# Performance work log

Hardware: AMD Instinct MI355X
Metric: run time of the kernel (lower is better)

Reference implementation:

```python
import jax, jax.numpy as jnp
import numpy as np

N_TOKENS = 16384
D_MODEL = 1024
N_SEG = 4
H_SEG = 1024  # intermediate_size (4096) // num_segments


def setup_inputs() -> dict:
    key = jax.random.key(0)
    kx, ki, kg, ku, kd = jax.random.split(key, 5)
    x = jax.random.normal(kx, (N_TOKENS, D_MODEL), dtype=jnp.float32)
    token_segment_indices = jax.random.randint(ki, (N_TOKENS,), 0, N_SEG, dtype=jnp.int64)
    s = 1.0 / np.sqrt(D_MODEL)
    # weights stored [seg, in, out] for x @ W
    gate_w = jax.random.normal(kg, (N_SEG, D_MODEL, H_SEG), dtype=jnp.float32) * s
    up_w = jax.random.normal(ku, (N_SEG, D_MODEL, H_SEG), dtype=jnp.float32) * s
    down_w = jax.random.normal(kd, (N_SEG, H_SEG, D_MODEL), dtype=jnp.float32) * (1.0 / np.sqrt(H_SEG))
    return {
        'x': x,
        'gate_w': gate_w,
        'up_w': up_w,
        'down_w': down_w,
        'token_segment_indices': token_segment_indices,
    }


def reference(x, gate_w, up_w, down_w, token_segment_indices):
    # _forward_with_indices: each token is processed only by its assigned
    # segment's SwiGLU FFN; all other contributions are zero.  We compute each
    # segment densely and mask (jit-friendly, same math as gather->ffn->scatter).
    out = jnp.zeros_like(x)
    for s in range(N_SEG):
        hidden = jax.nn.silu(x @ gate_w[s]) * (x @ up_w[s])  # [N, H_SEG]
        y = hidden @ down_w[s]                                # [N, D_MODEL]
        mask = (token_segment_indices == s)[:, None]
        out = out + jnp.where(mask, y, 0.0)
    return out
```

## Files before the change

kernel.cpp:

```cpp
#include <hip/hip_runtime.h>
#include <hip/hip_bf16.h>
#include <math.h>

#define NT   16384
#define DM   1024
#define NSEG 4
#define BK   64
#define HS   1024

typedef __attribute__((ext_vector_type(8))) short bf16x8;
typedef __attribute__((ext_vector_type(4))) float f32x4;

typedef __attribute__((address_space(1))) unsigned int gu32;
typedef __attribute__((address_space(3))) unsigned int lu32;

__device__ __forceinline__ void gll16(const void* g, void* l) {
  __builtin_amdgcn_global_load_lds((gu32*)(unsigned long long)g,
                                   (lu32*)(unsigned int)(unsigned long long)l,
                                   16, 0, 0);
}

__device__ __forceinline__ unsigned short cvt_bf16(float f) {
  unsigned int u = __float_as_uint(f);
  u += 0x7fffu + ((u >> 16) & 1u);
  return (unsigned short)(u >> 16);
}


__global__ void k_init(int* meta) {
  if (threadIdx.x < 16) meta[threadIdx.x] = 0;
}

__global__ void k_detect(const int* __restrict__ idx32, int* meta) {
  int t = blockIdx.x * 256 + threadIdx.x;
  int lane = threadIdx.x & 63;
  unsigned long long m = __ballot(idx32[2 * t + 1] != 0);
  if (lane == 0 && m) atomicOr(&meta[4], 1);
}

__global__ void k_count(const int* __restrict__ idx, int* meta) {
  int t = blockIdx.x * 256 + threadIdx.x;
  int s = meta[4] ? idx[t] : idx[2 * t];
  int lane = threadIdx.x & 63;
#pragma unroll
  for (int q = 0; q < 4; ++q) {
    unsigned long long m = __ballot(s == q);
    if (lane == 0 && m) atomicAdd(&meta[q], (int)__popcll(m));
  }
}

__global__ void k_base(int* meta) {
  int c0 = meta[0], c1 = meta[1], c2 = meta[2];
  meta[5] = 0; meta[6] = c0; meta[7] = c0 + c1; meta[8] = c0 + c1 + c2;
  meta[9] = 0; meta[10] = c0; meta[11] = c0 + c1; meta[12] = c0 + c1 + c2;
}

__global__ void k_rank(const int* __restrict__ idx, int* meta,
                       int* __restrict__ rank, int* __restrict__ perm) {
  int t = blockIdx.x * 256 + threadIdx.x;
  int s = meta[4] ? idx[t] : idx[2 * t];
  int lane = threadIdx.x & 63;
  unsigned long long lt = (1ull << lane) - 1;
#pragma unroll
  for (int q = 0; q < 4; ++q) {
    unsigned long long m = __ballot(s == q);
    int wb = 0;
    if (lane == 0 && m) wb = atomicAdd(&meta[9 + q], (int)__popcll(m));
    wb = __shfl(wb, 0);
    if (s == q) {
      int r = wb + (int)__popcll(m & lt);
      rank[t] = r;
      perm[r] = t;
    }
  }
}

__global__ __launch_bounds__(256) void k_cvt_x(const float4* __restrict__ x,
                                               const int* __restrict__ rank,
                                               uint4* __restrict__ xc) {
  int tid = threadIdx.x;
  int tok = blockIdx.x * 2 + (tid >> 7);
  int li = tid & 127;
  int r = rank[tok];
  float4 a = x[tok * 256 + li * 2];
  float4 b = x[tok * 256 + li * 2 + 1];
  uint4 o;
  o.x = cvt_bf16(a.x) | ((unsigned)cvt_bf16(a.y) << 16);
  o.y = cvt_bf16(a.z) | ((unsigned)cvt_bf16(a.w) << 16);
  o.z = cvt_bf16(b.x) | ((unsigned)cvt_bf16(b.y) << 16);
  o.w = cvt_bf16(b.z) | ((unsigned)cvt_bf16(b.w) << 16);
  xc[r * 128 + li] = o;
}

__global__ __launch_bounds__(256) void k_trans_w(
    const float* __restrict__ gw, const float* __restrict__ uw, const float* __restrict__ dw,
    unsigned short* __restrict__ gwt, unsigned short* __restrict__ uwt,
    unsigned short* __restrict__ dwt) {
  __shared__ float tile[64][65];
  int z = blockIdx.z, mtx = z >> 2, s = z & 3;
  const float* src = (mtx == 0 ? gw : mtx == 1 ? uw : dw) + (size_t)s * DM * HS;
  unsigned short* dst = (mtx == 0 ? gwt : mtx == 1 ? uwt : dwt) + (size_t)s * DM * HS;
  int k0 = blockIdx.y * 64, n0 = blockIdx.x * 64;
  int col = threadIdx.x & 63, rb = threadIdx.x >> 6;
#pragma unroll
  for (int i = 0; i < 64; i += 4)
    tile[i + rb][col] = src[(size_t)(k0 + i + rb) * 1024 + n0 + col];
  __syncthreads();
  int kp = threadIdx.x & 31, nb = threadIdx.x >> 5;
#pragma unroll
  for (int j = 0; j < 64; j += 8) {
    int nn = j + nb;
    unsigned int w = (unsigned)cvt_bf16(tile[2 * kp][nn]) |
                     ((unsigned)cvt_bf16(tile[2 * kp + 1][nn]) << 16);
    *(unsigned int*)(dst + (size_t)(n0 + nn) * 1024 + k0 + 2 * kp) = w;
  }
}

__global__ __launch_bounds__(256) void k_gateup(
    const unsigned short* __restrict__ xc,
    const unsigned short* __restrict__ gwt,
    const unsigned short* __restrict__ uwt,
    const int* __restrict__ meta,
    unsigned short* __restrict__ hidden) {
  const int seg = blockIdx.z;
  const int count = meta[seg];
  const int m0 = blockIdx.y * 128;
  if (m0 >= count) return;
  const int base = meta[5 + seg];
  const int n0 = blockIdx.x * 64;

  __shared__ __align__(16) unsigned short As[128 * BK];
  __shared__ __align__(16) unsigned short Bg[64 * BK];
  __shared__ __align__(16) unsigned short Bu[64 * BK];

  const int tid = threadIdx.x;
  const int lane = tid & 63;
  const int wave = tid >> 6;

  int a_off[4];
#pragma unroll
  for (int is = 0; is < 4; ++is) {
    int c = is * 256 + tid;
    int m = c >> 3;
    int kb = (c & 7) ^ (m & 7);
    int row = m0 + m;
    row = row < count ? row : count - 1;
    a_off[is] = (base + row) * DM + kb * 8;
  }
  int b_off[2];
#pragma unroll
  for (int is = 0; is < 2; ++is) {
    int c = is * 256 + tid;
    int n = c >> 3;
    int kb = (c & 7) ^ (n & 7);
    b_off[is] = (seg * HS + n0 + n) * DM + kb * 8;
  }

  f32x4 accg[4][2] = {};
  f32x4 accu[4][2] = {};
  const int wm = (wave & 1) * 64;
  const int wn = (wave >> 1) * 32;
  const int fm = lane & 15;
  const int fq = lane >> 4;
  const int fx = lane & 7;

  for (int kt = 0; kt < DM / BK; ++kt) {
    const int k0 = kt * BK;
    __syncthreads();
#pragma unroll
    for (int is = 0; is < 4; ++is)
      gll16(xc + a_off[is] + k0, (char*)As + (is * 256 + wave * 64) * 16);
#pragma unroll
    for (int is = 0; is < 2; ++is) {
      gll16(gwt + b_off[is] + k0, (char*)Bg + (is * 256 + wave * 64) * 16);
      gll16(uwt + b_off[is] + k0, (char*)Bu + (is * 256 + wave * 64) * 16);
    }
    __syncthreads();
#pragma unroll
    for (int s = 0; s < 2; ++s) {
      bf16x8 af[4], bgf[2], buf_[2];
      const int kb = (s * 4 + fq) ^ fx;
#pragma unroll
      for (int mi = 0; mi < 4; ++mi)
        af[mi] = *(const bf16x8*)((const char*)As + (((wm + mi * 16 + fm) * 8) + kb) * 16);
#pragma unroll
      for (int ni = 0; ni < 2; ++ni) {
        bgf[ni] = *(const bf16x8*)((const char*)Bg + (((wn + ni * 16 + fm) * 8) + kb) * 16);
        buf_[ni] = *(const bf16x8*)((const char*)Bu + (((wn + ni * 16 + fm) * 8) + kb) * 16);
      }
#pragma unroll
      for (int mi = 0; mi < 4; ++mi)
#pragma unroll
        for (int ni = 0; ni < 2; ++ni) {
          accg[mi][ni] = __builtin_amdgcn_mfma_f32_16x16x32_bf16(af[mi], bgf[ni], accg[mi][ni], 0, 0, 0);
          accu[mi][ni] = __builtin_amdgcn_mfma_f32_16x16x32_bf16(af[mi], buf_[ni], accu[mi][ni], 0, 0, 0);
        }
    }
  }

  const int rq = fq * 4;
#pragma unroll
  for (int mi = 0; mi < 4; ++mi) {
#pragma unroll
    for (int r = 0; r < 4; ++r) {
      int row = m0 + wm + mi * 16 + rq + r;
      if (row < count) {
        unsigned short* h = hidden + (size_t)(base + row) * HS + n0 + wn;
#pragma unroll
        for (int ni = 0; ni < 2; ++ni) {
          float g = accg[mi][ni][r];
          float u = accu[mi][ni][r];
          float sig = 1.0f / (1.0f + __expf(-g));
          h[ni * 16 + fm] = cvt_bf16(g * sig * u);
        }
      }
    }
  }
}

__global__ __launch_bounds__(256) void k_down(
    const unsigned short* __restrict__ hidden,
    const unsigned short* __restrict__ dwt,
    const int* __restrict__ meta,
    const int* __restrict__ perm,
    float* __restrict__ out) {
  const int seg = blockIdx.z;
  const int count = meta[seg];
  const int m0 = blockIdx.y * 128;
  if (m0 >= count) return;
  const int base = meta[5 + seg];
  const int n0 = blockIdx.x * 128;

  __shared__ __align__(16) unsigned short As[128 * BK];
  __shared__ __align__(16) unsigned short Bs[128 * BK];

  const int tid = threadIdx.x;
  const int lane = tid & 63;
  const int wave = tid >> 6;

  int a_off[4], b_off[4];
#pragma unroll
  for (int is = 0; is < 4; ++is) {
    int c = is * 256 + tid;
    int m = c >> 3;
    int kb = (c & 7) ^ (m & 7);
    int row = m0 + m;
    row = row < count ? row : count - 1;
    a_off[is] = (base + row) * HS + kb * 8;
    b_off[is] = (seg * DM + n0 + m) * HS + kb * 8;
  }

  f32x4 acc[4][4] = {};
  const int wm = (wave & 1) * 64;
  const int wn = (wave >> 1) * 64;
  const int fm = lane & 15;
  const int fq = lane >> 4;
  const int fx = lane & 7;

  for (int kt = 0; kt < HS / BK; ++kt) {
    const int k0 = kt * BK;
    __syncthreads();
#pragma unroll
    for (int is = 0; is < 4; ++is) {
      gll16(hidden + a_off[is] + k0, (char*)As + (is * 256 + wave * 64) * 16);
      gll16(dwt + b_off[is] + k0, (char*)Bs + (is * 256 + wave * 64) * 16);
    }
    __syncthreads();
#pragma unroll
    for (int s = 0; s < 2; ++s) {
      bf16x8 af[4], bf[4];
      const int kb = (s * 4 + fq) ^ fx;
#pragma unroll
      for (int mi = 0; mi < 4; ++mi)
        af[mi] = *(const bf16x8*)((const char*)As + (((wm + mi * 16 + fm) * 8) + kb) * 16);
#pragma unroll
      for (int ni = 0; ni < 4; ++ni)
        bf[ni] = *(const bf16x8*)((const char*)Bs + (((wn + ni * 16 + fm) * 8) + kb) * 16);
#pragma unroll
      for (int mi = 0; mi < 4; ++mi)
#pragma unroll
        for (int ni = 0; ni < 4; ++ni)
          acc[mi][ni] = __builtin_amdgcn_mfma_f32_16x16x32_bf16(af[mi], bf[ni], acc[mi][ni], 0, 0, 0);
    }
  }

  const int rq = fq * 4;
#pragma unroll
  for (int mi = 0; mi < 4; ++mi) {
#pragma unroll
    for (int r = 0; r < 4; ++r) {
      int row = m0 + wm + mi * 16 + rq + r;
      if (row < count) {
        int t = perm[base + row];
        float* o = out + (size_t)t * DM + n0 + wn;
#pragma unroll
        for (int ni = 0; ni < 4; ++ni)
          o[ni * 16 + fm] = acc[mi][ni][r];
      }
    }
  }
}


extern "C" void kernel_launch(void* const* d_in, const int* in_sizes, int n_in,
                              void* d_out, int out_size, void* d_ws, size_t ws_size,
                              hipStream_t stream) {
  const float* x  = (const float*)d_in[0];
  const float* gw = (const float*)d_in[1];
  const float* uw = (const float*)d_in[2];
  const float* dw = (const float*)d_in[3];
  const int* tsi  = (const int*)d_in[4];
  float* out = (float*)d_out;

  char* ws = (char*)d_ws;
  int* meta = (int*)ws;
  int* rank = (int*)(ws + 1024);
  int* perm = (int*)(ws + 1024 + NT * 4);
  unsigned short* xc  = (unsigned short*)(ws + (1 << 19));
  unsigned short* gwt = xc + (size_t)NT * DM;
  unsigned short* uwt = gwt + (size_t)NSEG * HS * DM;
  unsigned short* dwt = uwt + (size_t)NSEG * HS * DM;
  unsigned short* hid = dwt + (size_t)NSEG * DM * HS;

  k_init<<<1, 64, 0, stream>>>(meta);
  k_detect<<<NT / 512, 256, 0, stream>>>(tsi, meta);
  k_count<<<NT / 256, 256, 0, stream>>>(tsi, meta);
  k_base<<<1, 1, 0, stream>>>(meta);
  k_rank<<<NT / 256, 256, 0, stream>>>(tsi, meta, rank, perm);
  k_cvt_x<<<NT / 2, 256, 0, stream>>>((const float4*)x, rank, (uint4*)xc);
  k_trans_w<<<dim3(16, 16, 12), 256, 0, stream>>>(gw, uw, dw, gwt, uwt, dwt);
  k_gateup<<<dim3(16, 128, 4), 256, 0, stream>>>(xc, gwt, uwt, meta, hid);
  k_down<<<dim3(8, 128, 4), 256, 0, stream>>>(hid, dwt, meta, perm, out);
}
```

Baseline: 337.6 us.

## Fuse routing kernels, use compact tile table, overlap down-weight transpose with gate/up GEMM

Replaces the init/detect/count/base kernels with a two-kernel scan that also builds a compact table of (segment, row-tile) entries. The gate/up and down GEMMs now launch only as many blocks as the table holds, instead of a full 128x4 grid where most blocks exit early. The x conversion and gate/up weight transposes are merged into one launch, and the down-weight transpose moves into the gate/up launch so it overlaps the GEMM. Loop addressing switches to incremented pointers with precomputed LDS offsets, at the cost of a serial single-thread table build and a larger LDS union in the gate/up kernel.

```diff
diff --git a/kernel.cpp b/kernel.cpp
--- a/kernel.cpp
+++ b/kernel.cpp
@@ -27,35 +27,52 @@
 }
 
 
-__global__ void k_init(int* meta) {
-  if (threadIdx.x < 16) meta[threadIdx.x] = 0;
-}
-
-__global__ void k_detect(const int* __restrict__ idx32, int* meta) {
-  int t = blockIdx.x * 256 + threadIdx.x;
-  int lane = threadIdx.x & 63;
-  unsigned long long m = __ballot(idx32[2 * t + 1] != 0);
-  if (lane == 0 && m) atomicOr(&meta[4], 1);
-}
-
-__global__ void k_count(const int* __restrict__ idx, int* meta) {
-  int t = blockIdx.x * 256 + threadIdx.x;
-  int s = meta[4] ? idx[t] : idx[2 * t];
-  int lane = threadIdx.x & 63;
+__global__ __launch_bounds__(256) void k_scan(const int* __restrict__ idx, int* __restrict__ part) {
+  __shared__ int c[9];
+  int tid = threadIdx.x;
+  if (tid < 9) c[tid] = 0;
+  __syncthreads();
+  int t = blockIdx.x * 256 + tid;
+  int w0 = idx[2 * t], w1 = idx[2 * t + 1];
+  int lane = tid & 63;
+  unsigned long long m;
 #pragma unroll
   for (int q = 0; q < 4; ++q) {
-    unsigned long long m = __ballot(s == q);
-    if (lane == 0 && m) atomicAdd(&meta[q], (int)__popcll(m));
-  }
-}
-
-__global__ void k_base(int* meta) {
-  int c0 = meta[0], c1 = meta[1], c2 = meta[2];
-  meta[5] = 0; meta[6] = c0; meta[7] = c0 + c1; meta[8] = c0 + c1 + c2;
-  meta[9] = 0; meta[10] = c0; meta[11] = c0 + c1; meta[12] = c0 + c1 + c2;
-}
-
-__global__ void k_rank(const int* __restrict__ idx, int* meta,
+    m = __ballot(w0 == q); if (lane == 0 && m) atomicAdd(&c[q], (int)__popcll(m));
+    m = __ballot(w1 == q); if (lane == 0 && m) atomicAdd(&c[4 + q], (int)__popcll(m));
+  }
+  m = __ballot(w1 != 0);
+  if (lane == 0 && m) atomicAdd(&c[8], 1);
+  __syncthreads();
+  if (tid < 9) part[blockIdx.x * 9 + tid] = c[tid];
+}
+
+__global__ void k_base(const int* __restrict__ part, int* __restrict__ meta, int2* __restrict__ table) {
+  __shared__ int c[9];
+  int t = threadIdx.x;
+  if (t < 9) {
+    int s = 0;
+    for (int b = 0; b < 32; ++b) s += part[b * 9 + t];
+    c[t] = s;
+  }
+  __syncthreads();
+  if (t == 0) {
+    int flag = (c[8] != 0);
+    meta[4] = flag;
+    int base = 0;
+    for (int s = 0; s < 4; ++s) {
+      int cnt = flag ? (c[s] + c[4 + s]) : c[s];
+      meta[s] = cnt; meta[5 + s] = base; meta[9 + s] = base;
+      base += cnt;
+    }
+    int nt = 0;
+    for (int s = 0; s < 4; ++s)
+      for (int m0 = 0; m0 < meta[s]; m0 += 128) table[nt++] = make_int2(s, m0);
+    for (; nt < 132; ++nt) table[nt] = make_int2(-1, 0);
+  }
+}
+
+__global__ void k_rank(const int* __restrict__ idx, int* __restrict__ meta,
                        int* __restrict__ rank, int* __restrict__ perm) {
   int t = blockIdx.x * 256 + threadIdx.x;
   int s = meta[4] ? idx[t] : idx[2 * t];
@@ -75,38 +92,37 @@
   }
 }
 
-__global__ __launch_bounds__(256) void k_cvt_x(const float4* __restrict__ x,
-                                               const int* __restrict__ rank,
-                                               uint4* __restrict__ xc) {
-  int tid = threadIdx.x;
-  int tok = blockIdx.x * 2 + (tid >> 7);
-  int li = tid & 127;
-  int r = rank[tok];
-  float4 a = x[tok * 256 + li * 2];
-  float4 b = x[tok * 256 + li * 2 + 1];
-  uint4 o;
-  o.x = cvt_bf16(a.x) | ((unsigned)cvt_bf16(a.y) << 16);
-  o.y = cvt_bf16(a.z) | ((unsigned)cvt_bf16(a.w) << 16);
-  o.z = cvt_bf16(b.x) | ((unsigned)cvt_bf16(b.y) << 16);
-  o.w = cvt_bf16(b.z) | ((unsigned)cvt_bf16(b.w) << 16);
-  xc[r * 128 + li] = o;
-}
-
-__global__ __launch_bounds__(256) void k_trans_w(
-    const float* __restrict__ gw, const float* __restrict__ uw, const float* __restrict__ dw,
-    unsigned short* __restrict__ gwt, unsigned short* __restrict__ uwt,
-    unsigned short* __restrict__ dwt) {
+__global__ __launch_bounds__(256) void k_prep(
+    const float4* __restrict__ x, const int* __restrict__ rank, uint4* __restrict__ xc,
+    const float* __restrict__ gw, const float* __restrict__ uw,
+    unsigned short* __restrict__ gwt, unsigned short* __restrict__ uwt) {
   __shared__ float tile[64][65];
-  int z = blockIdx.z, mtx = z >> 2, s = z & 3;
-  const float* src = (mtx == 0 ? gw : mtx == 1 ? uw : dw) + (size_t)s * DM * HS;
-  unsigned short* dst = (mtx == 0 ? gwt : mtx == 1 ? uwt : dwt) + (size_t)s * DM * HS;
-  int k0 = blockIdx.y * 64, n0 = blockIdx.x * 64;
-  int col = threadIdx.x & 63, rb = threadIdx.x >> 6;
+  int bid = blockIdx.x, tid = threadIdx.x;
+  if (bid < 8192) {
+    int tok = bid * 2 + (tid >> 7);
+    int li = tid & 127;
+    int r = rank[tok];
+    float4 a = x[tok * 256 + li * 2];
+    float4 b = x[tok * 256 + li * 2 + 1];
+    uint4 o;
+    o.x = cvt_bf16(a.x) | ((unsigned)cvt_bf16(a.y) << 16);
+    o.y = cvt_bf16(a.z) | ((unsigned)cvt_bf16(a.w) << 16);
+    o.z = cvt_bf16(b.x) | ((unsigned)cvt_bf16(b.y) << 16);
+    o.w = cvt_bf16(b.z) | ((unsigned)cvt_bf16(b.w) << 16);
+    xc[r * 128 + li] = o;
+    return;
+  }
+  int tb = bid - 8192;
+  int mtx = tb >> 10, seg = (tb >> 8) & 3, tl = tb & 255;
+  const float* src = (mtx == 0 ? gw : uw) + (size_t)seg * DM * HS;
+  unsigned short* dst = (mtx == 0 ? gwt : uwt) + (size_t)seg * DM * HS;
+  int n0 = (tl & 15) * 64, k0 = (tl >> 4) * 64;
+  int col = tid & 63, rb = tid >> 6;
 #pragma unroll
   for (int i = 0; i < 64; i += 4)
     tile[i + rb][col] = src[(size_t)(k0 + i + rb) * 1024 + n0 + col];
   __syncthreads();
-  int kp = threadIdx.x & 31, nb = threadIdx.x >> 5;
+  int kp = tid & 31, nb = tid >> 5;
 #pragma unroll
   for (int j = 0; j < 64; j += 8) {
     int nn = j + nb;
@@ -121,23 +137,49 @@
     const unsigned short* __restrict__ gwt,
     const unsigned short* __restrict__ uwt,
     const int* __restrict__ meta,
+    const int2* __restrict__ table,
+    const float* __restrict__ dw,
+    unsigned short* __restrict__ dwt,
     unsigned short* __restrict__ hidden) {
-  const int seg = blockIdx.z;
-  const int count = meta[seg];
-  const int m0 = blockIdx.y * 128;
-  if (m0 >= count) return;
-  const int base = meta[5 + seg];
-  const int n0 = blockIdx.x * 64;
-
-  __shared__ __align__(16) unsigned short As[128 * BK];
-  __shared__ __align__(16) unsigned short Bg[64 * BK];
-  __shared__ __align__(16) unsigned short Bu[64 * BK];
-
-  const int tid = threadIdx.x;
+  union Sm {
+    struct { unsigned short As[128 * BK], Bg[64 * BK], Bu[64 * BK]; } g;
+    float tile[64][65];
+  };
+  __shared__ Sm sm;
+  const int bid = blockIdx.x, tid = threadIdx.x;
+
+  if (bid < 1024) {
+    int seg = bid >> 8, tl = bid & 255;
+    int n0t = (tl & 15) * 64, k0t = (tl >> 4) * 64;
+    const float* src = dw + (size_t)seg * DM * HS;
+    unsigned short* dst = dwt + (size_t)seg * DM * HS;
+    int col = tid & 63, rb = tid >> 6;
+#pragma unroll
+    for (int i = 0; i < 64; i += 4)
+      sm.tile[i + rb][col] = src[(size_t)(k0t + i + rb) * 1024 + n0t + col];
+    __syncthreads();
+    int kp = tid & 31, nb = tid >> 5;
+#pragma unroll
+    for (int j = 0; j < 64; j += 8) {
+      int nn = j + nb;
+      unsigned int w = (unsigned)cvt_bf16(sm.tile[2 * kp][nn]) |
+                       ((unsigned)cvt_bf16(sm.tile[2 * kp + 1][nn]) << 16);
+      *(unsigned int*)(dst + (size_t)(n0t + nn) * 1024 + k0t + 2 * kp) = w;
+    }
+    return;
+  }
+
+  const int g = bid - 1024;
+  const int2 te = table[g >> 4];
+  if (te.x < 0) return;
+  const int seg = te.x, m0 = te.y;
+  const int count = meta[seg], base = meta[5 + seg];
+  const int n0 = (g & 15) * 64;
+
   const int lane = tid & 63;
   const int wave = tid >> 6;
 
-  int a_off[4];
+  const unsigned short* ap[4];
 #pragma unroll
   for (int is = 0; is < 4; ++is) {
     int c = is * 256 + tid;
@@ -145,15 +187,16 @@
     int kb = (c & 7) ^ (m & 7);
     int row = m0 + m;
     row = row < count ? row : count - 1;
-    a_off[is] = (base + row) * DM + kb * 8;
-  }
-  int b_off[2];
+    ap[is] = xc + (size_t)(base + row) * DM + kb * 8;
+  }
+  const unsigned short *gp[2], *up[2];
 #pragma unroll
   for (int is = 0; is < 2; ++is) {
     int c = is * 256 + tid;
     int n = c >> 3;
     int kb = (c & 7) ^ (n & 7);
-    b_off[is] = (seg * HS + n0 + n) * DM + kb * 8;
+    gp[is] = gwt + (size_t)(seg * HS + n0 + n) * DM + kb * 8;
+    up[is] = uwt + (size_t)(seg * HS + n0 + n) * DM + kb * 8;
   }
 
   f32x4 accg[4][2] = {};
@@ -163,37 +206,45 @@
   const int fm = lane & 15;
   const int fq = lane >> 4;
   const int fx = lane & 7;
+  const int a_e0 = (wm + fm) * 64 + ((fq) ^ fx) * 8;
+  const int a_e1 = (wm + fm) * 64 + ((4 + fq) ^ fx) * 8;
+  const int b_e0 = (wn + fm) * 64 + ((fq) ^ fx) * 8;
+  const int b_e1 = (wn + fm) * 64 + ((4 + fq) ^ fx) * 8;
 
   for (int kt = 0; kt < DM / BK; ++kt) {
-    const int k0 = kt * BK;
     __syncthreads();
 #pragma unroll
     for (int is = 0; is < 4; ++is)
-      gll16(xc + a_off[is] + k0, (char*)As + (is * 256 + wave * 64) * 16);
+      gll16(ap[is], (char*)sm.g.As + (is * 256 + wave * 64) * 16);
 #pragma unroll
     for (int is = 0; is < 2; ++is) {
-      gll16(gwt + b_off[is] + k0, (char*)Bg + (is * 256 + wave * 64) * 16);
-      gll16(uwt + b_off[is] + k0, (char*)Bu + (is * 256 + wave * 64) * 16);
-    }
+      gll16(gp[is], (char*)sm.g.Bg + (is * 256 + wave * 64) * 16);
+      gll16(up[is], (char*)sm.g.Bu + (is * 256 + wave * 64) * 16);
+    }
+#pragma unroll
+    for (int is = 0; is < 4; ++is) ap[is] += BK;
+#pragma unroll
+    for (int is = 0; is < 2; ++is) { gp[is] += BK; up[is] += BK; }
     __syncthreads();
 #pragma unroll
     for (int s = 0; s < 2; ++s) {
-      bf16x8 af[4], bgf[2], buf_[2];
-      const int kb = (s * 4 + fq) ^ fx;
+      const unsigned short* Ap = sm.g.As + (s ? a_e1 : a_e0);
+      const unsigned short* Gp = sm.g.Bg + (s ? b_e1 : b_e0);
+      const unsigned short* Up = sm.g.Bu + (s ? b_e1 : b_e0);
+      bf16x8 af[4], bg2[2], bu2[2];
+#pragma unroll
+      for (int mi = 0; mi < 4; ++mi) af[mi] = *(const bf16x8*)(Ap + mi * 1024);
+#pragma unroll
+      for (int ni = 0; ni < 2; ++ni) {
+        bg2[ni] = *(const bf16x8*)(Gp + ni * 1024);
+        bu2[ni] = *(const bf16x8*)(Up + ni * 1024);
+      }
 #pragma unroll
       for (int mi = 0; mi < 4; ++mi)
-        af[mi] = *(const bf16x8*)((const char*)As + (((wm + mi * 16 + fm) * 8) + kb) * 16);
-#pragma unroll
-      for (int ni = 0; ni < 2; ++ni) {
-        bgf[ni] = *(const bf16x8*)((const char*)Bg + (((wn + ni * 16 + fm) * 8) + kb) * 16);
-        buf_[ni] = *(const bf16x8*)((const char*)Bu + (((wn + ni * 16 + fm) * 8) + kb) * 16);
-      }
-#pragma unroll
-      for (int mi = 0; mi < 4; ++mi)
 #pragma unroll
         for (int ni = 0; ni < 2; ++ni) {
-          accg[mi][ni] = __builtin_amdgcn_mfma_f32_16x16x32_bf16(af[mi], bgf[ni], accg[mi][ni], 0, 0, 0);
-          accu[mi][ni] = __builtin_amdgcn_mfma_f32_16x16x32_bf16(af[mi], buf_[ni], accu[mi][ni], 0, 0, 0);
+          accg[mi][ni] = __builtin_amdgcn_mfma_f32_16x16x32_bf16(af[mi], bg2[ni], accg[mi][ni], 0, 0, 0);
+          accu[mi][ni] = __builtin_amdgcn_mfma_f32_16x16x32_bf16(af[mi], bu2[ni], accu[mi][ni], 0, 0, 0);
         }
     }
   }
@@ -208,10 +259,10 @@
         unsigned short* h = hidden + (size_t)(base + row) * HS + n0 + wn;
 #pragma unroll
         for (int ni = 0; ni < 2; ++ni) {
-          float g = accg[mi][ni][r];
-          float u = accu[mi][ni][r];
-          float sig = 1.0f / (1.0f + __expf(-g));
-          h[ni * 16 + fm] = cvt_bf16(g * sig * u);
+          float gv = accg[mi][ni][r];
+          float uv = accu[mi][ni][r];
+          float sig = 1.0f / (1.0f + __expf(-gv));
+          h[ni * 16 + fm] = cvt_bf16(gv * sig * uv);
         }
       }
     }
@@ -222,23 +273,22 @@
     const unsigned short* __restrict__ hidden,
     const unsigned short* __restrict__ dwt,
     const int* __restrict__ meta,
+    const int2* __restrict__ table,
     const int* __restrict__ perm,
     float* __restrict__ out) {
-  const int seg = blockIdx.z;
-  const int count = meta[seg];
-  const int m0 = blockIdx.y * 128;
-  if (m0 >= count) return;
-  const int base = meta[5 + seg];
-  const int n0 = blockIdx.x * 128;
-
   __shared__ __align__(16) unsigned short As[128 * BK];
   __shared__ __align__(16) unsigned short Bs[128 * BK];
-
-  const int tid = threadIdx.x;
+  const int bid = blockIdx.x, tid = threadIdx.x;
+  const int2 te = table[bid >> 3];
+  if (te.x < 0) return;
+  const int seg = te.x, m0 = te.y;
+  const int count = meta[seg], base = meta[5 + seg];
+  const int n0 = (bid & 7) * 128;
+
   const int lane = tid & 63;
   const int wave = tid >> 6;
 
-  int a_off[4], b_off[4];
+  const unsigned short *ap[4], *bp[4];
 #pragma unroll
   for (int is = 0; is < 4; ++is) {
     int c = is * 256 + tid;
@@ -246,8 +296,8 @@
     int kb = (c & 7) ^ (m & 7);
     int row = m0 + m;
     row = row < count ? row : count - 1;
-    a_off[is] = (base + row) * HS + kb * 8;
-    b_off[is] = (seg * DM + n0 + m) * HS + kb * 8;
+    ap[is] = hidden + (size_t)(base + row) * HS + kb * 8;
+    bp[is] = dwt + (size_t)(seg * DM + n0 + m) * HS + kb * 8;
   }
 
   f32x4 acc[4][4] = {};
@@ -256,26 +306,30 @@
   const int fm = lane & 15;
   const int fq = lane >> 4;
   const int fx = lane & 7;
+  const int a_e0 = (wm + fm) * 64 + ((fq) ^ fx) * 8;
+  const int a_e1 = (wm + fm) * 64 + ((4 + fq) ^ fx) * 8;
+  const int b_e0 = (wn + fm) * 64 + ((fq) ^ fx) * 8;
+  const int b_e1 = (wn + fm) * 64 + ((4 + fq) ^ fx) * 8;
 
   for (int kt = 0; kt < HS / BK; ++kt) {
-    const int k0 = kt * BK;
     __syncthreads();
 #pragma unroll
     for (int is = 0; is < 4; ++is) {
-      gll16(hidden + a_off[is] + k0, (char*)As + (is * 256 + wave * 64) * 16);
-      gll16(dwt + b_off[is] + k0, (char*)Bs + (is * 256 + wave * 64) * 16);
-    }
+      gll16(ap[is], (char*)As + (is * 256 + wave * 64) * 16);
+      gll16(bp[is], (char*)Bs + (is * 256 + wave * 64) * 16);
+    }
+#pragma unroll
+    for (int is = 0; is < 4; ++is) { ap[is] += BK; bp[is] += BK; }
     __syncthreads();
 #pragma unroll
     for (int s = 0; s < 2; ++s) {
+      const unsigned short* Ap = As + (s ? a_e1 : a_e0);
+      const unsigned short* Bp = Bs + (s ? b_e1 : b_e0);
       bf16x8 af[4], bf[4];
-      const int kb = (s * 4 + fq) ^ fx;
-#pragma unroll
-      for (int mi = 0; mi < 4; ++mi)
-        af[mi] = *(const bf16x8*)((const char*)As + (((wm + mi * 16 + fm) * 8) + kb) * 16);
-#pragma unroll
-      for (int ni = 0; ni < 4; ++ni)
-        bf[ni] = *(const bf16x8*)((const char*)Bs + (((wn + ni * 16 + fm) * 8) + kb) * 16);
+#pragma unroll
+      for (int mi = 0; mi < 4; ++mi) af[mi] = *(const bf16x8*)(Ap + mi * 1024);
+#pragma unroll
+      for (int ni = 0; ni < 4; ++ni) bf[ni] = *(const bf16x8*)(Bp + ni * 1024);
 #pragma unroll
       for (int mi = 0; mi < 4; ++mi)
 #pragma unroll
@@ -313,22 +367,21 @@
   float* out = (float*)d_out;
 
   char* ws = (char*)d_ws;
-  int* meta = (int*)ws;
-  int* rank = (int*)(ws + 1024);
-  int* perm = (int*)(ws + 1024 + NT * 4);
-  unsigned short* xc  = (unsigned short*)(ws + (1 << 19));
+  int* meta  = (int*)ws;
+  int* part  = (int*)(ws + 256);
+  int2* table = (int2*)(ws + 2048);
+  int* rank  = (int*)(ws + 4096);
+  int* perm  = (int*)(ws + 4096 + NT * 4);
+  unsigned short* xc  = (unsigned short*)(ws + (1 << 18));
   unsigned short* gwt = xc + (size_t)NT * DM;
   unsigned short* uwt = gwt + (size_t)NSEG * HS * DM;
   unsigned short* dwt = uwt + (size_t)NSEG * HS * DM;
   unsigned short* hid = dwt + (size_t)NSEG * DM * HS;
 
-  k_init<<<1, 64, 0, stream>>>(meta);
-  k_detect<<<NT / 512, 256, 0, stream>>>(tsi, meta);
-  k_count<<<NT / 256, 256, 0, stream>>>(tsi, meta);
-  k_base<<<1, 1, 0, stream>>>(meta);
+  k_scan<<<32, 256, 0, stream>>>(tsi, part);
+  k_base<<<1, 64, 0, stream>>>(part, meta, table);
   k_rank<<<NT / 256, 256, 0, stream>>>(tsi, meta, rank, perm);
-  k_cvt_x<<<NT / 2, 256, 0, stream>>>((const float4*)x, rank, (uint4*)xc);
-  k_trans_w<<<dim3(16, 16, 12), 256, 0, stream>>>(gw, uw, dw, gwt, uwt, dwt);
-  k_gateup<<<dim3(16, 128, 4), 256, 0, stream>>>(xc, gwt, uwt, meta, hid);
-  k_down<<<dim3(8, 128, 4), 256, 0, stream>>>(hid, dwt, meta, perm, out);
-}
+  k_prep<<<8192 + 2048, 256, 0, stream>>>((const float4*)x, rank, (uint4*)xc, gw, uw, gwt, uwt);
+  k_gateup<<<1024 + 16 * 132, 256, 0, stream>>>(xc, gwt, uwt, meta, table, dw, dwt, hid);
+  k_down<<<8 * 132, 256, 0, stream>>>(hid, dwt, meta, table, perm, out);
+}
```

Result: no change. 334.2 us (-1.0%).
